# Kernel tuning notes

Measured on AMD Instinct MI355X. Metric: run time of the kernel, lower is better.

The kernel has to match this reference:

```python
import jax, jax.numpy as jnp
import numpy as np

SCALE = 0.5
DROP_P = 0.2

def setup_inputs() -> dict:
    key = jax.random.key(0)
    k1, k2 = jax.random.split(key)
    x1 = jax.random.normal(k1, (8, 2048, 128), dtype=jnp.float32)
    x2 = jax.random.normal(k2, (8, 2048, 128), dtype=jnp.float32)
    return {"x1": x1, "x2": x2}

def reference(x1, x2):
    # scores: [B, M, N] = x1 @ x2^T, scaled by 0.5
    scores = jnp.einsum('bmd,bnd->bmn', x1, x2) * SCALE
    probs = jax.nn.softmax(scores, axis=-1)
    # dropout p=0.2 (training mode in the torch source); fixed key for determinism
    keep = jax.random.bernoulli(jax.random.key(42), 1.0 - DROP_P, probs.shape)
    probs = jnp.where(keep, probs / (1.0 - DROP_P), 0.0)
    # out: [B, M, D] = probs @ x2
    return jnp.einsum('bmn,bnd->bmd', probs, x2)
```

## Files before the change

kernel.cpp:

```cpp
#include <hip/hip_runtime.h>
#include <stdint.h>


typedef __bf16 bf16x8 __attribute__((ext_vector_type(8)));
typedef float f32x4 __attribute__((ext_vector_type(4)));

__device__ __forceinline__ uint32_t rotl32(uint32_t x, uint32_t r) {
  return (x << r) | (x >> (32u - r));
}

__device__ __forceinline__ void threefry2x32_k42(uint32_t in0, uint32_t in1,
                                                 uint32_t& o0, uint32_t& o1) {
  const uint32_t ks0 = 0u;
  const uint32_t ks1 = 42u;
  const uint32_t ks2 = 0x1BD11BDAu ^ 0u ^ 42u;
  uint32_t x0 = in0 + ks0;
  uint32_t x1 = in1 + ks1;
#define TFR(r) { x0 += x1; x1 = rotl32(x1, r); x1 ^= x0; }
  TFR(13u) TFR(15u) TFR(26u) TFR(6u)
  x0 += ks1; x1 += ks2 + 1u;
  TFR(17u) TFR(29u) TFR(16u) TFR(24u)
  x0 += ks2; x1 += ks0 + 2u;
  TFR(13u) TFR(15u) TFR(26u) TFR(6u)
  x0 += ks0; x1 += ks1 + 3u;
  TFR(17u) TFR(29u) TFR(16u) TFR(24u)
  x0 += ks1; x1 += ks2 + 4u;
  TFR(13u) TFR(15u) TFR(26u) TFR(6u)
  x0 += ks2; x1 += ks0 + 5u;
#undef TFR
  o0 = x0; o1 = x1;
}

__device__ __forceinline__ uint32_t pack_bf16(float a, float b) {
  __bf16 ba = (__bf16)a;
  __bf16 bb = (__bf16)b;
  uint32_t ua = (uint32_t)__builtin_bit_cast(uint16_t, ba);
  uint32_t ub = (uint32_t)__builtin_bit_cast(uint16_t, bb);
  return ua | (ub << 16);
}

#define KEEP_LT 3435974144u
#define MBIAS 40.0f

__launch_bounds__(256, 4)
__global__ void prep_kernel(const float* __restrict__ x2,
                            uint4* __restrict__ KF,
                            uint4* __restrict__ VF) {
  const int tid = threadIdx.x;
  const int w = tid >> 6;
  const int lane = tid & 63;
  const int l15 = lane & 15;
  const int g = lane >> 4;
  const int T = blockIdx.x;
  const int b = blockIdx.y;
  const float* xb = x2 + (size_t)b * 2048 * 128;

  #pragma unroll
  for (int h = 0; h < 2; ++h) {
    const int n = T * 32 + h * 16 + l15;
    const float* p = xb + (size_t)n * 128 + w * 32 + 8 * g;
    float4 f0 = *(const float4*)(p);
    float4 f1 = *(const float4*)(p + 4);
    uint4 u;
    u.x = pack_bf16(f0.x, f0.y);
    u.y = pack_bf16(f0.z, f0.w);
    u.z = pack_bf16(f1.x, f1.y);
    u.w = pack_bf16(f1.z, f1.w);
    KF[(size_t)((b * 64 + T) * 8 + w * 2 + h) * 64 + lane] = u;
  }

  #pragma unroll
  for (int i = 0; i < 2; ++i) {
    const int dt = w + 4 * i;
    const int d = dt * 16 + l15;
    const float* p = xb + (size_t)(T * 32 + 8 * g) * 128 + d;
    uint4 u;
    u.x = pack_bf16(p[0],   p[128]);
    u.y = pack_bf16(p[256], p[384]);
    u.z = pack_bf16(p[512], p[640]);
    u.w = pack_bf16(p[768], p[896]);
    VF[(size_t)((b * 64 + T) * 8 + dt) * 64 + lane] = u;
  }
}

__launch_bounds__(512, 4)
__global__ void attn6_kernel(const float* __restrict__ x1,
                             const uint4* __restrict__ KF,
                             const uint4* __restrict__ VF,
                             float* __restrict__ out) {
  __shared__ __attribute__((aligned(16))) uint32_t SMEM[8832];

  const int tid = threadIdx.x;
  const int w = __builtin_amdgcn_readfirstlane(tid >> 6);
  const int lane = tid & 63;
  const int l15 = lane & 15;
  const int g = lane >> 4;
  const int q = w & 3;
  const int hs = w >> 2;
  const int id = blockIdx.y * 64 + blockIdx.x;
  const int b = id & 7;
  const int mt = id >> 3;
  const int m0 = mt * 32;

  uint32_t* Qld = &SMEM[0];
  uint32_t* PbW = &SMEM[2048 + w * 320];

  const float QSCALE = 0.5f * 1.44269504088896340736f;
  if (q == 0) {
    const float* qp_base =
        x1 + ((size_t)b * 2048 + m0 + hs * 16 + l15) * 128;
    #pragma unroll
    for (int c = 0; c < 4; ++c) {
      const float* qp = qp_base + c * 32 + g * 8;
      float4 f0 = *(const float4*)(qp);
      float4 f1 = *(const float4*)(qp + 4);
      uint4 u;
      u.x = pack_bf16(f0.x * QSCALE, f0.y * QSCALE);
      u.y = pack_bf16(f0.z * QSCALE, f0.w * QSCALE);
      u.z = pack_bf16(f1.x * QSCALE, f1.y * QSCALE);
      u.w = pack_bf16(f1.z * QSCALE, f1.w * QSCALE);
      *(uint4*)&Qld[hs * 1024 + (c * 64 + lane) * 4] = u;
    }
  }
  __syncthreads();

  f32x4 o[8];
  #pragma unroll
  for (int dt = 0; dt < 8; ++dt) o[dt] = (f32x4){0.f, 0.f, 0.f, 0.f};
  float lsum = 0.f;

  const uint32_t rbg = (uint32_t)b * 4194304u +
                       (uint32_t)(m0 + hs * 16 + l15) * 2048u +
                       (uint32_t)(q * 512) + (uint32_t)(4 * g);

  const uint4* kfp = KF + (size_t)((b * 64 + q * 16) * 8) * 64 + lane;
  const uint4* vfp = VF + (size_t)((b * 64 + q * 16) * 8) * 64 + lane;

  for (int tile = 0; tile < 16; ++tile) {
    f32x4 sa[2];
    sa[0] = (f32x4){0.f, 0.f, 0.f, 0.f};
    sa[1] = (f32x4){0.f, 0.f, 0.f, 0.f};
    __builtin_amdgcn_s_setprio(1);
    #pragma unroll
    for (int c = 0; c < 4; ++c) {
      bf16x8 qc = __builtin_bit_cast(
          bf16x8, *(const uint4*)&Qld[hs * 1024 + (c * 64 + lane) * 4]);
      bf16x8 k0 = __builtin_bit_cast(bf16x8, kfp[(c * 2 + 0) * 64]);
      bf16x8 k1 = __builtin_bit_cast(bf16x8, kfp[(c * 2 + 1) * 64]);
      sa[0] = __builtin_amdgcn_mfma_f32_16x16x32_bf16(k0, qc, sa[0], 0, 0, 0);
      sa[1] = __builtin_amdgcn_mfma_f32_16x16x32_bf16(k1, qc, sa[1], 0, 0, 0);
    }
    __builtin_amdgcn_s_setprio(0);

    #pragma unroll
    for (int t = 0; t < 2; ++t) {
      float p0 = __builtin_amdgcn_exp2f(sa[t][0]);
      float p1 = __builtin_amdgcn_exp2f(sa[t][1]);
      float p2 = __builtin_amdgcn_exp2f(sa[t][2]);
      float p3 = __builtin_amdgcn_exp2f(sa[t][3]);
      lsum += (p0 + p1) + (p2 + p3);
      const uint32_t ib = rbg + (uint32_t)(tile * 32 + t * 16);
      uint32_t h0, h1, bits;
      threefry2x32_k42(0u, ib + 0u, h0, h1); bits = h0 ^ h1;
      float q0 = (bits < KEEP_LT) ? p0 : 0.0f;
      threefry2x32_k42(0u, ib + 1u, h0, h1); bits = h0 ^ h1;
      float q1 = (bits < KEEP_LT) ? p1 : 0.0f;
      threefry2x32_k42(0u, ib + 2u, h0, h1); bits = h0 ^ h1;
      float q2 = (bits < KEEP_LT) ? p2 : 0.0f;
      threefry2x32_k42(0u, ib + 3u, h0, h1); bits = h0 ^ h1;
      float q3 = (bits < KEEP_LT) ? p3 : 0.0f;
      *(uint2*)&PbW[l15 * 20 + t * 8 + 2 * g] =
          make_uint2(pack_bf16(q0, q1), pack_bf16(q2, q3));
    }
    asm volatile("s_waitcnt lgkmcnt(0)" ::: "memory");
    uint4 pu = *(const uint4*)&PbW[l15 * 20 + 4 * g];
    bf16x8 pav = __builtin_bit_cast(bf16x8, pu);

    __builtin_amdgcn_s_setprio(1);
    #pragma unroll
    for (int dt = 0; dt < 8; ++dt) {
      bf16x8 vb = __builtin_bit_cast(bf16x8, vfp[dt * 64]);
      o[dt] = __builtin_amdgcn_mfma_f32_16x16x32_bf16(pav, vb, o[dt], 0, 0, 0);
    }
    __builtin_amdgcn_s_setprio(0);

    kfp += 512;
    vfp += 512;
    __syncthreads();
  }

  float* EP = (float*)&SMEM[0];
  float* EPL = EP + 8192;
  #pragma unroll
  for (int pass = 0; pass < 2; ++pass) {
    if (pass == 1) __syncthreads();
    if (hs == pass) {
      EPL[l15 * 36 + q * 4 + g] = lsum;
      #pragma unroll
      for (int dt = 0; dt < 8; ++dt)
        #pragma unroll
        for (int r = 0; r < 4; ++r)
          EP[((q * 8 + dt) * 4 + r) * 64 + lane] = o[dt][r];
    }
    __syncthreads();
    float scale[4];
    #pragma unroll
    for (int r = 0; r < 4; ++r) {
      const float4* lp = (const float4*)&EPL[(4 * g + r) * 36];
      float4 A = lp[0], B4 = lp[1], C4 = lp[2], D4 = lp[3];
      float L = ((A.x + A.y) + (A.z + A.w)) + ((B4.x + B4.y) + (B4.z + B4.w)) +
                ((C4.x + C4.y) + (C4.z + C4.w)) + ((D4.x + D4.y) + (D4.z + D4.w));
      scale[r] = 1.0f / (L * 0.8f);
    }
    #pragma unroll
    for (int r = 0; r < 4; ++r) {
      const int base = (w * 4 + r) * 64 + lane;
      float tot = EP[base] + EP[base + 2048] + EP[base + 4096] + EP[base + 6144];
      out[((size_t)b * 2048 + m0 + pass * 16 + 4 * g + r) * 128 + w * 16 + l15] =
          tot * scale[r];
    }
  }
}

union FragAB {
  bf16x8 v;
  uint32_t u[4];
};

__launch_bounds__(256, 2)
__global__ void attn_kernel(const float* __restrict__ x1,
                            const float* __restrict__ x2,
                            float* __restrict__ out) {
  __shared__ __attribute__((aligned(16))) uint32_t SMEM[4][4800];

  const int tid = threadIdx.x;
  const int wv = __builtin_amdgcn_readfirstlane(tid >> 6);
  const int lane = tid & 63;
  const int l15 = lane & 15;
  const int g = lane >> 4;
  const int b = blockIdx.y;
  const int m0 = blockIdx.x * 32;

  uint32_t* KtW = &SMEM[wv][0];
  uint32_t* VtW = &SMEM[wv][2176];
  uint32_t* PbW = &SMEM[wv][4480];

  const float QSCALE = 0.5f * 1.44269504088896340736f;
  FragAB qf[2][4];
  #pragma unroll
  for (int s = 0; s < 2; ++s) {
    const float* qp_base = x1 + ((size_t)b * 2048 + m0 + s * 16 + l15) * 128;
    #pragma unroll
    for (int c = 0; c < 4; ++c) {
      const float* qp = qp_base + c * 32 + g * 8;
      float4 f0 = *(const float4*)(qp);
      float4 f1 = *(const float4*)(qp + 4);
      qf[s][c].u[0] = pack_bf16(f0.x * QSCALE, f0.y * QSCALE);
      qf[s][c].u[1] = pack_bf16(f0.z * QSCALE, f0.w * QSCALE);
      qf[s][c].u[2] = pack_bf16(f1.x * QSCALE, f1.y * QSCALE);
      qf[s][c].u[3] = pack_bf16(f1.z * QSCALE, f1.w * QSCALE);
    }
  }

  f32x4 o[2][8];
  #pragma unroll
  for (int s = 0; s < 2; ++s)
    #pragma unroll
    for (int dt = 0; dt < 8; ++dt) o[s][dt] = (f32x4){0.f, 0.f, 0.f, 0.f};
  float lsum[2] = {0.f, 0.f};

  uint32_t rb[2];
  #pragma unroll
  for (int s = 0; s < 2; ++s)
    rb[s] = (uint32_t)b * 4194304u +
            (uint32_t)(m0 + s * 16 + l15) * 2048u + (uint32_t)(wv * 512);

  const float4* x2b4 = (const float4*)(x2 + (size_t)b * 2048 * 128);
  const uint32_t permsel = (l15 & 1) ? 0x07060302u : 0x05040100u;

  for (int tile = 0; tile < 16; ++tile) {
    const int n0g = wv * 512 + tile * 32;

    #pragma unroll
    for (int i = 0; i < 16; ++i) {
      int n = 2 * i + (lane >> 5);
      int dq = lane & 31;
      float4 v = x2b4[(size_t)(n0g + n) * 32 + dq];
      uint32_t p0 = pack_bf16(v.x, v.y);
      uint32_t p1 = pack_bf16(v.z, v.w);
      *(uint2*)&KtW[n * 68 + 2 * dq] = make_uint2(p0, p1);
      VtW[dq * 36 + n] = p0;
      VtW[(dq + 32) * 36 + n] = p1;
    }
    asm volatile("s_waitcnt lgkmcnt(0)" ::: "memory");

    f32x4 sa[2][2];
    #pragma unroll
    for (int s = 0; s < 2; ++s)
      #pragma unroll
      for (int t = 0; t < 2; ++t) sa[s][t] = (f32x4){0.f, 0.f, 0.f, 0.f};
    #pragma unroll
    for (int c = 0; c < 4; ++c) {
      FragAB k0, k1;
      uint4 a0 = *(const uint4*)&KtW[l15 * 68 + c * 16 + 4 * g];
      uint4 a1 = *(const uint4*)&KtW[(16 + l15) * 68 + c * 16 + 4 * g];
      k0.u[0] = a0.x; k0.u[1] = a0.y; k0.u[2] = a0.z; k0.u[3] = a0.w;
      k1.u[0] = a1.x; k1.u[1] = a1.y; k1.u[2] = a1.z; k1.u[3] = a1.w;
      sa[0][0] = __builtin_amdgcn_mfma_f32_16x16x32_bf16(k0.v, qf[0][c].v, sa[0][0], 0, 0, 0);
      sa[0][1] = __builtin_amdgcn_mfma_f32_16x16x32_bf16(k1.v, qf[0][c].v, sa[0][1], 0, 0, 0);
      sa[1][0] = __builtin_amdgcn_mfma_f32_16x16x32_bf16(k0.v, qf[1][c].v, sa[1][0], 0, 0, 0);
      sa[1][1] = __builtin_amdgcn_mfma_f32_16x16x32_bf16(k1.v, qf[1][c].v, sa[1][1], 0, 0, 0);
    }

    FragAB pa[2];
    #pragma unroll
    for (int s = 0; s < 2; ++s) {
      #pragma unroll
      for (int t = 0; t < 2; ++t) {
        float p0 = __builtin_amdgcn_exp2f(sa[s][t][0] - MBIAS);
        float p1 = __builtin_amdgcn_exp2f(sa[s][t][1] - MBIAS);
        float p2 = __builtin_amdgcn_exp2f(sa[s][t][2] - MBIAS);
        float p3 = __builtin_amdgcn_exp2f(sa[s][t][3] - MBIAS);
        lsum[s] += (p0 + p1) + (p2 + p3);
        uint32_t ib = rb[s] + (uint32_t)(tile * 32 + t * 16 + 4 * g);
        uint32_t h0, h1, bits;
        threefry2x32_k42(0u, ib + 0u, h0, h1); bits = h0 ^ h1;
        float q0 = (bits < KEEP_LT) ? p0 : 0.0f;
        threefry2x32_k42(0u, ib + 1u, h0, h1); bits = h0 ^ h1;
        float q1 = (bits < KEEP_LT) ? p1 : 0.0f;
        threefry2x32_k42(0u, ib + 2u, h0, h1); bits = h0 ^ h1;
        float q2 = (bits < KEEP_LT) ? p2 : 0.0f;
        threefry2x32_k42(0u, ib + 3u, h0, h1); bits = h0 ^ h1;
        float q3 = (bits < KEEP_LT) ? p3 : 0.0f;
        *(uint2*)&PbW[l15 * 20 + t * 8 + 2 * g] =
            make_uint2(pack_bf16(q0, q1), pack_bf16(q2, q3));
      }
      asm volatile("s_waitcnt lgkmcnt(0)" ::: "memory");
      uint4 pu = *(const uint4*)&PbW[l15 * 20 + 4 * g];
      pa[s].u[0] = pu.x; pa[s].u[1] = pu.y; pa[s].u[2] = pu.z; pa[s].u[3] = pu.w;
    }

    #pragma unroll
    for (int dt = 0; dt < 8; ++dt) {
      int rowp = ((l15 >> 1) & 1) * 32 + 4 * dt + (l15 >> 2);
      const uint32_t* vr = &VtW[rowp * 36 + 8 * g];
      uint4 U0 = *(const uint4*)vr;
      uint4 U1 = *(const uint4*)(vr + 4);
      FragAB vb;
      vb.u[0] = __builtin_amdgcn_perm(U0.y, U0.x, permsel);
      vb.u[1] = __builtin_amdgcn_perm(U0.w, U0.z, permsel);
      vb.u[2] = __builtin_amdgcn_perm(U1.y, U1.x, permsel);
      vb.u[3] = __builtin_amdgcn_perm(U1.w, U1.z, permsel);
      o[0][dt] = __builtin_amdgcn_mfma_f32_16x16x32_bf16(pa[0].v, vb.v, o[0][dt], 0, 0, 0);
      o[1][dt] = __builtin_amdgcn_mfma_f32_16x16x32_bf16(pa[1].v, vb.v, o[1][dt], 0, 0, 0);
    }
  }

  __syncthreads();
  float* EP = (float*)&SMEM[0][0];
  #pragma unroll
  for (int s = 0; s < 2; ++s) {
    #pragma unroll
    for (int dt = 0; dt < 8; ++dt)
      #pragma unroll
      for (int r = 0; r < 4; ++r)
        EP[(((wv * 2 + s) * 8 + dt) * 4 + r) * 64 + lane] = o[s][dt][r];
    EP[16384 + (s * 16 + l15) * 16 + wv * 4 + g] = lsum[s];
  }
  __syncthreads();
  const int s = wv >> 1;
  float scale[4];
  #pragma unroll
  for (int r = 0; r < 4; ++r) {
    const float4* lp = (const float4*)&EP[16384 + (s * 16 + 4 * g + r) * 16];
    float4 A = lp[0], B4 = lp[1], C4 = lp[2], D4 = lp[3];
    float L = ((A.x + A.y) + (A.z + A.w)) + ((B4.x + B4.y) + (B4.z + B4.w)) +
              ((C4.x + C4.y) + (C4.z + C4.w)) + ((D4.x + D4.y) + (D4.z + D4.w));
    scale[r] = 1.0f / (L * 0.8f);
  }
  #pragma unroll
  for (int it = 0; it < 4; ++it) {
    int dt = (wv * 4 + it) & 7;
    #pragma unroll
    for (int r = 0; r < 4; ++r) {
      int base = ((s * 8 + dt) * 4 + r) * 64 + lane;
      float tot = EP[base] + EP[base + 4096] + EP[base + 8192] + EP[base + 12288];
      out[((size_t)b * 2048 + m0 + s * 16 + 4 * g + r) * 128 + dt * 16 + l15] =
          tot * scale[r];
    }
  }
}

extern "C" void kernel_launch(void* const* d_in, const int* in_sizes, int n_in,
                              void* d_out, int out_size, void* d_ws, size_t ws_size,
                              hipStream_t stream) {
  const float* x1 = (const float*)d_in[0];
  const float* x2 = (const float*)d_in[1];
  float* out = (float*)d_out;
  if (d_ws != nullptr && ws_size >= (size_t)8 * 1024 * 1024) {
    uint4* KF = (uint4*)d_ws;
    uint4* VF = KF + 262144;
    prep_kernel<<<dim3(64, 8, 1), dim3(256, 1, 1), 0, stream>>>(x2, KF, VF);
    attn6_kernel<<<dim3(64, 8, 1), dim3(512, 1, 1), 0, stream>>>(x1, KF, VF, out);
  } else {
    attn_kernel<<<dim3(64, 8, 1), dim3(256, 1, 1), 0, stream>>>(x1, x2, out);
  }
}
```

Before: 174.6 us.

## Use 4 waves each handling both query halves with register-resident Q and staggered tiles

Replaces the 8-wave block (two half-row groups of 4 waves) with a 4-wave block in which each wave computes both 16-row query slices. Q fragments now live in registers instead of LDS, and each K/V fragment is reused for two MFMAs, halving global K/V fragment loads per output. The per-tile __syncthreads is removed and each wave starts at a different key tile offset, which spreads cache access. In exchange, per-wave register use doubles (two sets of accumulators), occupancy bounds drop, and the threefry/exp work per wave doubles.

Measured after the change: 153.0 us. 12.4% less time.

```diff
diff --git a/kernel.cpp b/kernel.cpp
--- a/kernel.cpp
+++ b/kernel.cpp
@@ -83,8 +83,8 @@
   }
 }
 
-__launch_bounds__(512, 4)
-__global__ void attn6_kernel(const float* __restrict__ x1,
+__launch_bounds__(256, 2)
+__global__ void attn7_kernel(const float* __restrict__ x1,
                              const uint4* __restrict__ KF,
                              const uint4* __restrict__ VF,
                              float* __restrict__ out) {
@@ -95,20 +95,19 @@
   const int lane = tid & 63;
   const int l15 = lane & 15;
   const int g = lane >> 4;
-  const int q = w & 3;
-  const int hs = w >> 2;
   const int id = blockIdx.y * 64 + blockIdx.x;
   const int b = id & 7;
   const int mt = id >> 3;
   const int m0 = mt * 32;
-
-  uint32_t* Qld = &SMEM[0];
-  uint32_t* PbW = &SMEM[2048 + w * 320];
+  const int t0 = (mt + w) & 15;
+
+  uint32_t* PbW = &SMEM[w * 640];
 
   const float QSCALE = 0.5f * 1.44269504088896340736f;
-  if (q == 0) {
-    const float* qp_base =
-        x1 + ((size_t)b * 2048 + m0 + hs * 16 + l15) * 128;
+  bf16x8 qf[2][4];
+  #pragma unroll
+  for (int s = 0; s < 2; ++s) {
+    const float* qp_base = x1 + ((size_t)b * 2048 + m0 + s * 16 + l15) * 128;
     #pragma unroll
     for (int c = 0; c < 4; ++c) {
       const float* qp = qp_base + c * 32 + g * 8;
@@ -119,89 +118,100 @@
       u.y = pack_bf16(f0.z * QSCALE, f0.w * QSCALE);
       u.z = pack_bf16(f1.x * QSCALE, f1.y * QSCALE);
       u.w = pack_bf16(f1.z * QSCALE, f1.w * QSCALE);
-      *(uint4*)&Qld[hs * 1024 + (c * 64 + lane) * 4] = u;
-    }
-  }
-  __syncthreads();
-
-  f32x4 o[8];
-  #pragma unroll
-  for (int dt = 0; dt < 8; ++dt) o[dt] = (f32x4){0.f, 0.f, 0.f, 0.f};
-  float lsum = 0.f;
-
-  const uint32_t rbg = (uint32_t)b * 4194304u +
-                       (uint32_t)(m0 + hs * 16 + l15) * 2048u +
-                       (uint32_t)(q * 512) + (uint32_t)(4 * g);
-
-  const uint4* kfp = KF + (size_t)((b * 64 + q * 16) * 8) * 64 + lane;
-  const uint4* vfp = VF + (size_t)((b * 64 + q * 16) * 8) * 64 + lane;
+      qf[s][c] = __builtin_bit_cast(bf16x8, u);
+    }
+  }
+
+  f32x4 o[2][8];
+  #pragma unroll
+  for (int s = 0; s < 2; ++s)
+    #pragma unroll
+    for (int dt = 0; dt < 8; ++dt) o[s][dt] = (f32x4){0.f, 0.f, 0.f, 0.f};
+  float lsum[2] = {0.f, 0.f};
+
+  uint32_t rb[2];
+  #pragma unroll
+  for (int s = 0; s < 2; ++s)
+    rb[s] = (uint32_t)b * 4194304u +
+            (uint32_t)(m0 + s * 16 + l15) * 2048u + (uint32_t)(w * 512) +
+            (uint32_t)(4 * g);
+
+  const uint4* kfb = KF + (size_t)((b * 64 + w * 16) * 8) * 64 + lane;
+  const uint4* vfb = VF + (size_t)((b * 64 + w * 16) * 8) * 64 + lane;
 
   for (int tile = 0; tile < 16; ++tile) {
-    f32x4 sa[2];
-    sa[0] = (f32x4){0.f, 0.f, 0.f, 0.f};
-    sa[1] = (f32x4){0.f, 0.f, 0.f, 0.f};
+    const int tt = (t0 + tile) & 15;
+    const uint4* kfp = kfb + (size_t)tt * 512;
+    const uint4* vfp = vfb + (size_t)tt * 512;
+
+    f32x4 sa[2][2];
+    #pragma unroll
+    for (int s = 0; s < 2; ++s) {
+      sa[s][0] = (f32x4){0.f, 0.f, 0.f, 0.f};
+      sa[s][1] = (f32x4){0.f, 0.f, 0.f, 0.f};
+    }
     __builtin_amdgcn_s_setprio(1);
     #pragma unroll
     for (int c = 0; c < 4; ++c) {
-      bf16x8 qc = __builtin_bit_cast(
-          bf16x8, *(const uint4*)&Qld[hs * 1024 + (c * 64 + lane) * 4]);
       bf16x8 k0 = __builtin_bit_cast(bf16x8, kfp[(c * 2 + 0) * 64]);
       bf16x8 k1 = __builtin_bit_cast(bf16x8, kfp[(c * 2 + 1) * 64]);
-      sa[0] = __builtin_amdgcn_mfma_f32_16x16x32_bf16(k0, qc, sa[0], 0, 0, 0);
-      sa[1] = __builtin_amdgcn_mfma_f32_16x16x32_bf16(k1, qc, sa[1], 0, 0, 0);
+      sa[0][0] = __builtin_amdgcn_mfma_f32_16x16x32_bf16(k0, qf[0][c], sa[0][0], 0, 0, 0);
+      sa[0][1] = __builtin_amdgcn_mfma_f32_16x16x32_bf16(k1, qf[0][c], sa[0][1], 0, 0, 0);
+      sa[1][0] = __builtin_amdgcn_mfma_f32_16x16x32_bf16(k0, qf[1][c], sa[1][0], 0, 0, 0);
+      sa[1][1] = __builtin_amdgcn_mfma_f32_16x16x32_bf16(k1, qf[1][c], sa[1][1], 0, 0, 0);
     }
     __builtin_amdgcn_s_setprio(0);
 
     #pragma unroll
-    for (int t = 0; t < 2; ++t) {
-      float p0 = __builtin_amdgcn_exp2f(sa[t][0]);
-      float p1 = __builtin_amdgcn_exp2f(sa[t][1]);
-      float p2 = __builtin_amdgcn_exp2f(sa[t][2]);
-      float p3 = __builtin_amdgcn_exp2f(sa[t][3]);
-      lsum += (p0 + p1) + (p2 + p3);
-      const uint32_t ib = rbg + (uint32_t)(tile * 32 + t * 16);
-      uint32_t h0, h1, bits;
-      threefry2x32_k42(0u, ib + 0u, h0, h1); bits = h0 ^ h1;
-      float q0 = (bits < KEEP_LT) ? p0 : 0.0f;
-      threefry2x32_k42(0u, ib + 1u, h0, h1); bits = h0 ^ h1;
-      float q1 = (bits < KEEP_LT) ? p1 : 0.0f;
-      threefry2x32_k42(0u, ib + 2u, h0, h1); bits = h0 ^ h1;
-      float q2 = (bits < KEEP_LT) ? p2 : 0.0f;
-      threefry2x32_k42(0u, ib + 3u, h0, h1); bits = h0 ^ h1;
-      float q3 = (bits < KEEP_LT) ? p3 : 0.0f;
-      *(uint2*)&PbW[l15 * 20 + t * 8 + 2 * g] =
-          make_uint2(pack_bf16(q0, q1), pack_bf16(q2, q3));
+    for (int s = 0; s < 2; ++s) {
+      #pragma unroll
+      for (int t = 0; t < 2; ++t) {
+        float p0 = __builtin_amdgcn_exp2f(sa[s][t][0]);
+        float p1 = __builtin_amdgcn_exp2f(sa[s][t][1]);
+        float p2 = __builtin_amdgcn_exp2f(sa[s][t][2]);
+        float p3 = __builtin_amdgcn_exp2f(sa[s][t][3]);
+        lsum[s] += (p0 + p1) + (p2 + p3);
+        const uint32_t ib = rb[s] + (uint32_t)(tt * 32 + t * 16);
+        uint32_t h0, h1, bits;
+        threefry2x32_k42(0u, ib + 0u, h0, h1); bits = h0 ^ h1;
+        float q0 = (bits < KEEP_LT) ? p0 : 0.0f;
+        threefry2x32_k42(0u, ib + 1u, h0, h1); bits = h0 ^ h1;
+        float q1 = (bits < KEEP_LT) ? p1 : 0.0f;
+        threefry2x32_k42(0u, ib + 2u, h0, h1); bits = h0 ^ h1;
+        float q2 = (bits < KEEP_LT) ? p2 : 0.0f;
+        threefry2x32_k42(0u, ib + 3u, h0, h1); bits = h0 ^ h1;
+        float q3 = (bits < KEEP_LT) ? p3 : 0.0f;
+        *(uint2*)&PbW[s * 320 + l15 * 20 + t * 8 + 2 * g] =
+            make_uint2(pack_bf16(q0, q1), pack_bf16(q2, q3));
+      }
     }
     asm volatile("s_waitcnt lgkmcnt(0)" ::: "memory");
-    uint4 pu = *(const uint4*)&PbW[l15 * 20 + 4 * g];
-    bf16x8 pav = __builtin_bit_cast(bf16x8, pu);
+    uint4 pu0 = *(const uint4*)&PbW[l15 * 20 + 4 * g];
+    uint4 pu1 = *(const uint4*)&PbW[320 + l15 * 20 + 4 * g];
+    bf16x8 pa0 = __builtin_bit_cast(bf16x8, pu0);
+    bf16x8 pa1 = __builtin_bit_cast(bf16x8, pu1);
 
     __builtin_amdgcn_s_setprio(1);
     #pragma unroll
     for (int dt = 0; dt < 8; ++dt) {
       bf16x8 vb = __builtin_bit_cast(bf16x8, vfp[dt * 64]);
-      o[dt] = __builtin_amdgcn_mfma_f32_16x16x32_bf16(pav, vb, o[dt], 0, 0, 0);
+      o[0][dt] = __builtin_amdgcn_mfma_f32_16x16x32_bf16(pa0, vb, o[0][dt], 0, 0, 0);
+      o[1][dt] = __builtin_amdgcn_mfma_f32_16x16x32_bf16(pa1, vb, o[1][dt], 0, 0, 0);
     }
     __builtin_amdgcn_s_setprio(0);
-
-    kfp += 512;
-    vfp += 512;
-    __syncthreads();
   }
 
   float* EP = (float*)&SMEM[0];
   float* EPL = EP + 8192;
   #pragma unroll
-  for (int pass = 0; pass < 2; ++pass) {
-    if (pass == 1) __syncthreads();
-    if (hs == pass) {
-      EPL[l15 * 36 + q * 4 + g] = lsum;
-      #pragma unroll
-      for (int dt = 0; dt < 8; ++dt)
-        #pragma unroll
-        for (int r = 0; r < 4; ++r)
-          EP[((q * 8 + dt) * 4 + r) * 64 + lane] = o[dt][r];
-    }
+  for (int s = 0; s < 2; ++s) {
+    __syncthreads();
+    EPL[l15 * 36 + w * 4 + g] = lsum[s];
+    #pragma unroll
+    for (int dt = 0; dt < 8; ++dt)
+      #pragma unroll
+      for (int r = 0; r < 4; ++r)
+        EP[((w * 8 + dt) * 4 + r) * 64 + lane] = o[s][dt][r];
     __syncthreads();
     float scale[4];
     #pragma unroll
@@ -213,11 +223,15 @@
       scale[r] = 1.0f / (L * 0.8f);
     }
     #pragma unroll
-    for (int r = 0; r < 4; ++r) {
-      const int base = (w * 4 + r) * 64 + lane;
-      float tot = EP[base] + EP[base + 2048] + EP[base + 4096] + EP[base + 6144];
-      out[((size_t)b * 2048 + m0 + pass * 16 + 4 * g + r) * 128 + w * 16 + l15] =
-          tot * scale[r];
+    for (int i = 0; i < 2; ++i) {
+      const int dt = w * 2 + i;
+      #pragma unroll
+      for (int r = 0; r < 4; ++r) {
+        int base = (dt * 4 + r) * 64 + lane;
+        float tot = EP[base] + EP[base + 2048] + EP[base + 4096] + EP[base + 6144];
+        out[((size_t)b * 2048 + m0 + s * 16 + 4 * g + r) * 128 + dt * 16 + l15] =
+            tot * scale[r];
+      }
     }
   }
 }
@@ -401,7 +415,7 @@
     uint4* KF = (uint4*)d_ws;
     uint4* VF = KF + 262144;
     prep_kernel<<<dim3(64, 8, 1), dim3(256, 1, 1), 0, stream>>>(x2, KF, VF);
-    attn6_kernel<<<dim3(64, 8, 1), dim3(512, 1, 1), 0, stream>>>(x1, KF, VF, out);
+    attn7_kernel<<<dim3(64, 8, 1), dim3(256, 1, 1), 0, stream>>>(x1, KF, VF, out);
   } else {
     attn_kernel<<<dim3(64, 8, 1), dim3(256, 1, 1), 0, stream>>>(x1, x2, out);
   }
```
